# Kernel optimization log

Measured on AMD Instinct MI355X. Metric: run time of the kernel, lower is better.

Reference implementation:

```python
import jax, jax.numpy as jnp
import numpy as np

N, DX, DZ, DY, H = 8192, 64, 128, 16, 512


def setup_inputs() -> dict:
    key = jax.random.key(0)
    ks = jax.random.split(key, 8)
    s1 = 1.0 / np.sqrt(DX)
    s2 = 1.0 / np.sqrt(H)
    return {
        "z_pred": jax.random.normal(ks[0], (N, DZ), dtype=jnp.float32),
        "x_label": jax.random.normal(ks[1], (N, DX), dtype=jnp.float32),
        "y_label": jax.random.normal(ks[2], (N, DY), dtype=jnp.float32),
        "W1": jax.random.normal(ks[3], (DX, H), dtype=jnp.float32) * s1,
        "b1": jnp.zeros((H,), dtype=jnp.float32),
        "W2": jax.random.normal(ks[4], (H, DZ), dtype=jnp.float32) * s2,
        "b2": jnp.zeros((DZ,), dtype=jnp.float32),
        "A": jax.random.normal(ks[5], (DZ, DZ), dtype=jnp.float32) * (1.0 / np.sqrt(DZ)),
        "B": jax.random.normal(ks[6], (DZ, DY), dtype=jnp.float32) * (1.0 / np.sqrt(DY)),
    }


def reference(z_pred, x_label, y_label, W1, b1, W2, b2, A, B):
    # forward_mapper T: x (dx,) -> (dz,), 2-layer tanh MLP
    def T(x):
        return jnp.tanh(x @ W1 + b1) @ W2 + b2

    # diff_eq: per-sample nonlinear dynamics x_dot = tanh(x)
    x_dot = jnp.tanh(x_label)  # (N, dx)

    # per-sample Jacobian dT/dx: (N, dz, dx). Equivalent to the torch code's
    # full N x N batched Jacobian followed by the diagonal slice, but without
    # the O(N^2) waste.
    jac = jax.vmap(jax.jacrev(T))(x_label)  # (N, dz, dx)

    dtdx_mul_f = jnp.einsum("nzd,nd->nz", jac, x_dot)  # (N, dz)
    m_mul_t = z_pred @ A.T                              # (N, dz)
    k_mul_h = y_label @ B.T                             # (N, dz)

    pde = dtdx_mul_f - m_mul_t - k_mul_h                # (N, dz)
    loss_batch = jnp.linalg.norm(pde, axis=1)           # (N,)
    return jnp.mean(loss_batch)
```

## Files before the change

kernel.cpp:

```cpp
#include <hip/hip_runtime.h>
#include <math.h>

#define Nn   8192
#define DXc  64
#define DZc  128
#define DYc  16
#define Hc   512
#define KCp  672
#define SSTR 72

typedef short bf16x8 __attribute__((ext_vector_type(8)));
typedef float f32x4  __attribute__((ext_vector_type(4)));

__device__ __forceinline__ float fast_tanh(float x) {
    float e = __expf(2.0f * x);
    return 1.0f - 2.0f / (e + 1.0f);
}
__device__ __forceinline__ short f2bf(float f) {
    unsigned u = __float_as_uint(f);
    return (short)((u + 0x7FFFu + ((u >> 16) & 1u)) >> 16);
}

__global__ void prep_kernel(const float* __restrict__ W1,
                            const float* __restrict__ W2,
                            const float* __restrict__ A,
                            const float* __restrict__ Bm,
                            short* __restrict__ W1T,
                            short* __restrict__ WcT) {
    int idx = blockIdx.x * 256 + threadIdx.x;
    if (idx < Hc * DXc) {
        int j = idx >> 6, k = idx & 63;
        W1T[idx] = f2bf(W1[k * Hc + j]);
    }
    int i2 = idx - Hc * DXc;
    if (i2 >= 0 && i2 < DZc * KCp) {
        int z = i2 / KCp, k = i2 - z * KCp;
        float v = 0.f;
        if (k < Hc)                  v =  W2[k * DZc + z];
        else if (k < Hc + DZc)       v = -A[z * DZc + (k - Hc)];
        else if (k < Hc + DZc + DYc) v = -Bm[z * DYc + (k - Hc - DZc)];
        WcT[i2] = f2bf(v);
    }
}

#define MFMA16(a, b, c) __builtin_amdgcn_mfma_f32_16x16x32_bf16((a), (b), (c), 0, 0, 0)

__global__ __launch_bounds__(256, 2)
void pde_main(const float* __restrict__ z_pred,
              const float* __restrict__ x_label,
              const float* __restrict__ y_label,
              const float* __restrict__ b1,
              const short* __restrict__ W1T,
              const short* __restrict__ WcT,
              float* __restrict__ partial) {
    __shared__ __align__(16) short sS[4][16 * SSTR];
    __shared__ float Pred[4][16][DZc];
    __shared__ float rsum[16];
    __shared__ float norms[16];

    const int tid  = threadIdx.x;
    const int w    = tid >> 6;
    const int lane = tid & 63;
    const int n16  = lane & 15;
    const int q    = lane >> 4;
    const int n0   = blockIdx.x * 16;

    if (tid < 16) rsum[tid] = 0.f;

    f32x4 accP[8];
#pragma unroll
    for (int zt = 0; zt < 8; zt++) accP[zt] = (f32x4){0.f, 0.f, 0.f, 0.f};

    const float4* xr4 = (const float4*)(x_label + (size_t)(n0 + n16) * DXc + q * 8);
    float4 x0 = xr4[0], x1 = xr4[1];
    float4 x2 = xr4[8], x3 = xr4[9];
    bf16x8 ax0, ax1, at0, at1;
    {
        const float* xa = (const float*)&x0;
        float v[16] = {x0.x,x0.y,x0.z,x0.w, x1.x,x1.y,x1.z,x1.w,
                       x2.x,x2.y,x2.z,x2.w, x3.x,x3.y,x3.z,x3.w};
        (void)xa;
#pragma unroll
        for (int i = 0; i < 8; i++) {
            ax0[i] = f2bf(v[i]);                ax1[i] = f2bf(v[8 + i]);
            at0[i] = f2bf(fast_tanh(v[i]));     at1[i] = f2bf(fast_tanh(v[8 + i]));
        }
    }

    short* sw = &sS[w][0];

#pragma unroll
    for (int cc = 0; cc < 2; cc++) {
        const int jbase = (w + cc * 4) * 64;
#pragma unroll
        for (int t = 0; t < 4; t++) {
            const int jt = jbase + t * 16;
            const short* bp = W1T + (size_t)(jt + n16) * DXc + q * 8;
            bf16x8 bw0 = *(const bf16x8*)bp;
            bf16x8 bw1 = *(const bf16x8*)(bp + 32);
            f32x4 h = (f32x4){0.f, 0.f, 0.f, 0.f};
            f32x4 u = (f32x4){0.f, 0.f, 0.f, 0.f};
            h = MFMA16(ax0, bw0, h);  h = MFMA16(ax1, bw1, h);
            u = MFMA16(at0, bw0, u);  u = MFMA16(at1, bw1, u);
            const float bj = b1[jt + n16];
#pragma unroll
            for (int reg = 0; reg < 4; reg++) {
                float tv = fast_tanh(h[reg] + bj);
                float s  = (1.f - tv * tv) * u[reg];
                sw[(q * 4 + reg) * SSTR + t * 16 + n16] = f2bf(s);
            }
        }
        bf16x8 sa0 = *(const bf16x8*)(sw + n16 * SSTR + q * 8);
        bf16x8 sa1 = *(const bf16x8*)(sw + n16 * SSTR + 32 + q * 8);
#pragma unroll
        for (int zt = 0; zt < 8; zt++) {
            const short* wp = WcT + (size_t)(zt * 16 + n16) * KCp + jbase + q * 8;
            bf16x8 w0 = *(const bf16x8*)wp;
            bf16x8 w1 = *(const bf16x8*)(wp + 32);
            accP[zt] = MFMA16(sa0, w0, accP[zt]);
            accP[zt] = MFMA16(sa1, w1, accP[zt]);
        }
    }

    if (w < 2) {
        const int kz = w * 64;
        const float4* zr4 = (const float4*)(z_pred + (size_t)(n0 + n16) * DZc + kz + q * 8);
        float4 z0 = zr4[0], z1 = zr4[1], z2 = zr4[8], z3 = zr4[9];
        float v[16] = {z0.x,z0.y,z0.z,z0.w, z1.x,z1.y,z1.z,z1.w,
                       z2.x,z2.y,z2.z,z2.w, z3.x,z3.y,z3.z,z3.w};
        bf16x8 az0, az1;
#pragma unroll
        for (int i = 0; i < 8; i++) { az0[i] = f2bf(v[i]); az1[i] = f2bf(v[8 + i]); }
        const int kb = Hc + kz;
#pragma unroll
        for (int zt = 0; zt < 8; zt++) {
            const short* wp = WcT + (size_t)(zt * 16 + n16) * KCp + kb + q * 8;
            bf16x8 w0 = *(const bf16x8*)wp;
            bf16x8 w1 = *(const bf16x8*)(wp + 32);
            accP[zt] = MFMA16(az0, w0, accP[zt]);
            accP[zt] = MFMA16(az1, w1, accP[zt]);
        }
    } else if (w == 2) {
        bf16x8 ay = (bf16x8){0,0,0,0,0,0,0,0};
        if (q < 2) {
            const float4* yr4 = (const float4*)(y_label + (size_t)(n0 + n16) * DYc + q * 8);
            float4 y0 = yr4[0], y1 = yr4[1];
            float v[8] = {y0.x,y0.y,y0.z,y0.w, y1.x,y1.y,y1.z,y1.w};
#pragma unroll
            for (int i = 0; i < 8; i++) ay[i] = f2bf(v[i]);
        }
        const int kb = Hc + DZc;
#pragma unroll
        for (int zt = 0; zt < 8; zt++) {
            const short* wp = WcT + (size_t)(zt * 16 + n16) * KCp + kb + q * 8;
            bf16x8 w0 = *(const bf16x8*)wp;
            accP[zt] = MFMA16(ay, w0, accP[zt]);
        }
    }

#pragma unroll
    for (int zt = 0; zt < 8; zt++)
#pragma unroll
        for (int reg = 0; reg < 4; reg++)
            Pred[w][q * 4 + reg][zt * 16 + n16] = accP[zt][reg];
    __syncthreads();

    {
        const int r = tid & 15, seg = tid >> 4;
        float ss = 0.f;
#pragma unroll
        for (int c8 = 0; c8 < 8; c8++) {
            int c = seg * 8 + c8;
            float v = Pred[0][r][c] + Pred[1][r][c] + Pred[2][r][c] + Pred[3][r][c];
            ss = fmaf(v, v, ss);
        }
        atomicAdd(&rsum[r], ss);
    }
    __syncthreads();
    if (tid < 16) norms[tid] = sqrtf(rsum[tid]);
    __syncthreads();
    if (tid == 0) {
        float s = 0.f;
#pragma unroll
        for (int i = 0; i < 16; i++) s += norms[i];
        partial[blockIdx.x] = s;
    }
}

__global__ void reduce_kernel(const float* __restrict__ partial, float* __restrict__ out) {
    __shared__ float s4[4];
    int tid = threadIdx.x;
    float v = partial[tid] + partial[tid + 256];
#pragma unroll
    for (int off = 32; off >= 1; off >>= 1) v += __shfl_down(v, off);
    if ((tid & 63) == 0) s4[tid >> 6] = v;
    __syncthreads();
    if (tid == 0) out[0] = (s4[0] + s4[1] + s4[2] + s4[3]) * (1.0f / (float)Nn);
}

extern "C" void kernel_launch(void* const* d_in, const int* in_sizes, int n_in,
                              void* d_out, int out_size, void* d_ws, size_t ws_size,
                              hipStream_t stream) {
    const float* z_pred  = (const float*)d_in[0];
    const float* x_label = (const float*)d_in[1];
    const float* y_label = (const float*)d_in[2];
    const float* W1      = (const float*)d_in[3];
    const float* b1      = (const float*)d_in[4];
    const float* W2      = (const float*)d_in[5];
    const float* A       = (const float*)d_in[7];
    const float* Bm      = (const float*)d_in[8];

    short* W1T = (short*)d_ws;
    short* WcT = W1T + Hc * DXc;
    float* partial = (float*)(WcT + DZc * KCp);

    const int prep_elems = Hc * DXc + DZc * KCp;
    prep_kernel<<<(prep_elems + 255) / 256, 256, 0, stream>>>(W1, W2, A, Bm, W1T, WcT);
    pde_main<<<Nn / 16, 256, 0, stream>>>(z_pred, x_label, y_label, b1, W1T, WcT, partial);
    reduce_kernel<<<1, 256, 0, stream>>>(partial, (float*)d_out);
}
```

Measured before the change: 87.06 us.

## Split output columns across waves and coalesce weight prep via shared-memory transpose

The main kernel now writes the full 16x512 sensitivity tile to one shared buffer and has each wave compute a 32-column slice of the output over the full K, instead of each wave doing a K-slice over all 128 columns. This removes the 4x partial-output shared buffer and its cross-wave reduction, and replaces it with a shuffle-based row sum of squares. The prep kernel is rewritten to transpose W1/W2 through shared memory with vectorized bf16x8 stores, in 25 blocks. The trade-off is an extra block-wide barrier before the second GEMM, and every wave now reads all of sS.

```diff
diff --git a/kernel.cpp b/kernel.cpp
--- a/kernel.cpp
+++ b/kernel.cpp
@@ -7,7 +7,7 @@
 #define DYc  16
 #define Hc   512
 #define KCp  672
-#define SSTR 72
+#define SSTR 520
 
 typedef short bf16x8 __attribute__((ext_vector_type(8)));
 typedef float f32x4  __attribute__((ext_vector_type(4)));
@@ -19,6 +19,12 @@
 __device__ __forceinline__ short f2bf(float f) {
     unsigned u = __float_as_uint(f);
     return (short)((u + 0x7FFFu + ((u >> 16) & 1u)) >> 16);
+}
+__device__ __forceinline__ bf16x8 pack8(float4 a, float4 b) {
+    bf16x8 r;
+    r[0]=f2bf(a.x); r[1]=f2bf(a.y); r[2]=f2bf(a.z); r[3]=f2bf(a.w);
+    r[4]=f2bf(b.x); r[5]=f2bf(b.y); r[6]=f2bf(b.z); r[7]=f2bf(b.w);
+    return r;
 }
 
 __global__ void prep_kernel(const float* __restrict__ W1,
@@ -27,19 +33,66 @@
                             const float* __restrict__ Bm,
                             short* __restrict__ W1T,
                             short* __restrict__ WcT) {
-    int idx = blockIdx.x * 256 + threadIdx.x;
-    if (idx < Hc * DXc) {
-        int j = idx >> 6, k = idx & 63;
-        W1T[idx] = f2bf(W1[k * Hc + j]);
-    }
-    int i2 = idx - Hc * DXc;
-    if (i2 >= 0 && i2 < DZc * KCp) {
-        int z = i2 / KCp, k = i2 - z * KCp;
-        float v = 0.f;
-        if (k < Hc)                  v =  W2[k * DZc + z];
-        else if (k < Hc + DZc)       v = -A[z * DZc + (k - Hc)];
-        else if (k < Hc + DZc + DYc) v = -Bm[z * DYc + (k - Hc - DZc)];
-        WcT[i2] = f2bf(v);
+    __shared__ float tile[64 * 129];
+    const int blk = blockIdx.x, t = threadIdx.x;
+
+    if (blk < 8) {
+        const int jb = blk * 64;
+#pragma unroll
+        for (int p = 0; p < 16; p++) {
+            int lin = p * 256 + t;
+            int k = lin >> 6, jj = lin & 63;
+            tile[jj * 65 + k] = W1[(size_t)k * Hc + jb + jj];
+        }
+        __syncthreads();
+#pragma unroll
+        for (int p = 0; p < 2; p++) {
+            int jj = p * 32 + (t >> 3), k8 = (t & 7) * 8;
+            bf16x8 v;
+#pragma unroll
+            for (int i = 0; i < 8; i++) v[i] = f2bf(tile[jj * 65 + k8 + i]);
+            *(bf16x8*)(W1T + (size_t)(jb + jj) * DXc + k8) = v;
+        }
+    } else if (blk < 16) {
+        const int kb = (blk - 8) * 64;
+#pragma unroll
+        for (int p = 0; p < 32; p++) {
+            int lin = p * 256 + t;
+            int kk = lin >> 7, z = lin & 127;
+            tile[kk * 129 + z] = W2[(size_t)(kb + kk) * DZc + z];
+        }
+        __syncthreads();
+#pragma unroll
+        for (int p = 0; p < 4; p++) {
+            int z = p * 32 + (t >> 3), k8 = (t & 7) * 8;
+            bf16x8 v;
+#pragma unroll
+            for (int i = 0; i < 8; i++) v[i] = f2bf(tile[(k8 + i) * 129 + z]);
+            *(bf16x8*)(WcT + (size_t)z * KCp + kb + k8) = v;
+        }
+    } else if (blk < 24) {
+        int idx8 = (blk - 16) * 256 + t;
+        int z = idx8 >> 4, c8 = (idx8 & 15) * 8;
+        float4 a0 = *(const float4*)(A + (size_t)z * DZc + c8);
+        float4 a1 = *(const float4*)(A + (size_t)z * DZc + c8 + 4);
+        bf16x8 v;
+        v[0]=f2bf(-a0.x); v[1]=f2bf(-a0.y); v[2]=f2bf(-a0.z); v[3]=f2bf(-a0.w);
+        v[4]=f2bf(-a1.x); v[5]=f2bf(-a1.y); v[6]=f2bf(-a1.z); v[7]=f2bf(-a1.w);
+        *(bf16x8*)(WcT + (size_t)z * KCp + Hc + c8) = v;
+    } else {
+#pragma unroll
+        for (int p = 0; p < 2; p++) {
+            int cid = p * 256 + t;
+            int z = cid >> 2, c8 = (cid & 3) * 8;
+            bf16x8 v = (bf16x8){0,0,0,0,0,0,0,0};
+            if (c8 < DYc) {
+                float4 b0 = *(const float4*)(Bm + (size_t)z * DYc + c8);
+                float4 b1 = *(const float4*)(Bm + (size_t)z * DYc + c8 + 4);
+                v[0]=f2bf(-b0.x); v[1]=f2bf(-b0.y); v[2]=f2bf(-b0.z); v[3]=f2bf(-b0.w);
+                v[4]=f2bf(-b1.x); v[5]=f2bf(-b1.y); v[6]=f2bf(-b1.z); v[7]=f2bf(-b1.w);
+            }
+            *(bf16x8*)(WcT + (size_t)z * KCp + Hc + DZc + c8) = v;
+        }
     }
 }
 
@@ -53,10 +106,8 @@
               const short* __restrict__ W1T,
               const short* __restrict__ WcT,
               float* __restrict__ partial) {
-    __shared__ __align__(16) short sS[4][16 * SSTR];
-    __shared__ float Pred[4][16][DZc];
+    __shared__ __align__(16) short sS[16 * SSTR];
     __shared__ float rsum[16];
-    __shared__ float norms[16];
 
     const int tid  = threadIdx.x;
     const int w    = tid >> 6;
@@ -67,39 +118,29 @@
 
     if (tid < 16) rsum[tid] = 0.f;
 
-    f32x4 accP[8];
-#pragma unroll
-    for (int zt = 0; zt < 8; zt++) accP[zt] = (f32x4){0.f, 0.f, 0.f, 0.f};
-
-    const float4* xr4 = (const float4*)(x_label + (size_t)(n0 + n16) * DXc + q * 8);
-    float4 x0 = xr4[0], x1 = xr4[1];
-    float4 x2 = xr4[8], x3 = xr4[9];
-    bf16x8 ax0, ax1, at0, at1;
+    const float* xp = x_label + (size_t)(n0 + n16) * DXc + q * 8;
+    float4 x0 = *(const float4*)xp,        x1 = *(const float4*)(xp + 4);
+    float4 x2 = *(const float4*)(xp + 32), x3 = *(const float4*)(xp + 36);
+    bf16x8 ax0 = pack8(x0, x1), ax1 = pack8(x2, x3);
+    bf16x8 at0, at1;
     {
-        const float* xa = (const float*)&x0;
         float v[16] = {x0.x,x0.y,x0.z,x0.w, x1.x,x1.y,x1.z,x1.w,
                        x2.x,x2.y,x2.z,x2.w, x3.x,x3.y,x3.z,x3.w};
-        (void)xa;
-#pragma unroll
-        for (int i = 0; i < 8; i++) {
-            ax0[i] = f2bf(v[i]);                ax1[i] = f2bf(v[8 + i]);
-            at0[i] = f2bf(fast_tanh(v[i]));     at1[i] = f2bf(fast_tanh(v[8 + i]));
-        }
-    }
-
-    short* sw = &sS[w][0];
+#pragma unroll
+        for (int i = 0; i < 8; i++) { at0[i] = f2bf(fast_tanh(v[i])); at1[i] = f2bf(fast_tanh(v[8 + i])); }
+    }
 
 #pragma unroll
     for (int cc = 0; cc < 2; cc++) {
-        const int jbase = (w + cc * 4) * 64;
+        const int jb = w * 128 + cc * 64;
 #pragma unroll
         for (int t = 0; t < 4; t++) {
-            const int jt = jbase + t * 16;
+            const int jt = jb + t * 16;
             const short* bp = W1T + (size_t)(jt + n16) * DXc + q * 8;
             bf16x8 bw0 = *(const bf16x8*)bp;
             bf16x8 bw1 = *(const bf16x8*)(bp + 32);
-            f32x4 h = (f32x4){0.f, 0.f, 0.f, 0.f};
-            f32x4 u = (f32x4){0.f, 0.f, 0.f, 0.f};
+            f32x4 h = (f32x4){0.f,0.f,0.f,0.f};
+            f32x4 u = (f32x4){0.f,0.f,0.f,0.f};
             h = MFMA16(ax0, bw0, h);  h = MFMA16(ax1, bw1, h);
             u = MFMA16(at0, bw0, u);  u = MFMA16(at1, bw1, u);
             const float bj = b1[jt + n16];
@@ -107,82 +148,73 @@
             for (int reg = 0; reg < 4; reg++) {
                 float tv = fast_tanh(h[reg] + bj);
                 float s  = (1.f - tv * tv) * u[reg];
-                sw[(q * 4 + reg) * SSTR + t * 16 + n16] = f2bf(s);
+                sS[(q * 4 + reg) * SSTR + jt + n16] = f2bf(s);
             }
         }
-        bf16x8 sa0 = *(const bf16x8*)(sw + n16 * SSTR + q * 8);
-        bf16x8 sa1 = *(const bf16x8*)(sw + n16 * SSTR + 32 + q * 8);
-#pragma unroll
-        for (int zt = 0; zt < 8; zt++) {
-            const short* wp = WcT + (size_t)(zt * 16 + n16) * KCp + jbase + q * 8;
-            bf16x8 w0 = *(const bf16x8*)wp;
-            bf16x8 w1 = *(const bf16x8*)(wp + 32);
-            accP[zt] = MFMA16(sa0, w0, accP[zt]);
-            accP[zt] = MFMA16(sa1, w1, accP[zt]);
-        }
-    }
-
-    if (w < 2) {
-        const int kz = w * 64;
-        const float4* zr4 = (const float4*)(z_pred + (size_t)(n0 + n16) * DZc + kz + q * 8);
-        float4 z0 = zr4[0], z1 = zr4[1], z2 = zr4[8], z3 = zr4[9];
-        float v[16] = {z0.x,z0.y,z0.z,z0.w, z1.x,z1.y,z1.z,z1.w,
-                       z2.x,z2.y,z2.z,z2.w, z3.x,z3.y,z3.z,z3.w};
-        bf16x8 az0, az1;
-#pragma unroll
-        for (int i = 0; i < 8; i++) { az0[i] = f2bf(v[i]); az1[i] = f2bf(v[8 + i]); }
-        const int kb = Hc + kz;
-#pragma unroll
-        for (int zt = 0; zt < 8; zt++) {
-            const short* wp = WcT + (size_t)(zt * 16 + n16) * KCp + kb + q * 8;
-            bf16x8 w0 = *(const bf16x8*)wp;
-            bf16x8 w1 = *(const bf16x8*)(wp + 32);
-            accP[zt] = MFMA16(az0, w0, accP[zt]);
-            accP[zt] = MFMA16(az1, w1, accP[zt]);
-        }
-    } else if (w == 2) {
+    }
+
+    const int z0r = w * 32;
+    const short* wr0 = WcT + (size_t)(z0r + n16) * KCp;
+    const short* wr1 = WcT + (size_t)(z0r + 16 + n16) * KCp;
+    f32x4 acc0 = (f32x4){0.f,0.f,0.f,0.f};
+    f32x4 acc1 = (f32x4){0.f,0.f,0.f,0.f};
+
+    {
+        const float* zp = z_pred + (size_t)(n0 + n16) * DZc + q * 8;
+#pragma unroll
+        for (int kc = 0; kc < 4; kc++) {
+            float4 a0 = *(const float4*)(zp + kc * 32);
+            float4 a1 = *(const float4*)(zp + kc * 32 + 4);
+            bf16x8 az = pack8(a0, a1);
+            bf16x8 b0 = *(const bf16x8*)(wr0 + Hc + kc * 32 + q * 8);
+            bf16x8 b1f = *(const bf16x8*)(wr1 + Hc + kc * 32 + q * 8);
+            acc0 = MFMA16(az, b0, acc0);
+            acc1 = MFMA16(az, b1f, acc1);
+        }
+    }
+    {
         bf16x8 ay = (bf16x8){0,0,0,0,0,0,0,0};
         if (q < 2) {
-            const float4* yr4 = (const float4*)(y_label + (size_t)(n0 + n16) * DYc + q * 8);
-            float4 y0 = yr4[0], y1 = yr4[1];
-            float v[8] = {y0.x,y0.y,y0.z,y0.w, y1.x,y1.y,y1.z,y1.w};
-#pragma unroll
-            for (int i = 0; i < 8; i++) ay[i] = f2bf(v[i]);
-        }
-        const int kb = Hc + DZc;
-#pragma unroll
-        for (int zt = 0; zt < 8; zt++) {
-            const short* wp = WcT + (size_t)(zt * 16 + n16) * KCp + kb + q * 8;
-            bf16x8 w0 = *(const bf16x8*)wp;
-            accP[zt] = MFMA16(ay, w0, accP[zt]);
-        }
-    }
-
-#pragma unroll
-    for (int zt = 0; zt < 8; zt++)
-#pragma unroll
-        for (int reg = 0; reg < 4; reg++)
-            Pred[w][q * 4 + reg][zt * 16 + n16] = accP[zt][reg];
+            const float* yp = y_label + (size_t)(n0 + n16) * DYc + q * 8;
+            float4 y0 = *(const float4*)yp, y1 = *(const float4*)(yp + 4);
+            ay = pack8(y0, y1);
+        }
+        bf16x8 b0 = *(const bf16x8*)(wr0 + Hc + DZc + q * 8);
+        bf16x8 b1f = *(const bf16x8*)(wr1 + Hc + DZc + q * 8);
+        acc0 = MFMA16(ay, b0, acc0);
+        acc1 = MFMA16(ay, b1f, acc1);
+    }
+
     __syncthreads();
 
-    {
-        const int r = tid & 15, seg = tid >> 4;
-        float ss = 0.f;
-#pragma unroll
-        for (int c8 = 0; c8 < 8; c8++) {
-            int c = seg * 8 + c8;
-            float v = Pred[0][r][c] + Pred[1][r][c] + Pred[2][r][c] + Pred[3][r][c];
-            ss = fmaf(v, v, ss);
-        }
-        atomicAdd(&rsum[r], ss);
+#pragma unroll
+    for (int kc = 0; kc < 16; kc++) {
+        bf16x8 sa = *(const bf16x8*)(sS + n16 * SSTR + kc * 32 + q * 8);
+        bf16x8 b0 = *(const bf16x8*)(wr0 + kc * 32 + q * 8);
+        bf16x8 b1f = *(const bf16x8*)(wr1 + kc * 32 + q * 8);
+        acc0 = MFMA16(sa, b0, acc0);
+        acc1 = MFMA16(sa, b1f, acc1);
+    }
+
+    float ss[4];
+#pragma unroll
+    for (int reg = 0; reg < 4; reg++) {
+        ss[reg] = fmaf(acc0[reg], acc0[reg], acc1[reg] * acc1[reg]);
+        ss[reg] += __shfl_xor(ss[reg], 1);
+        ss[reg] += __shfl_xor(ss[reg], 2);
+        ss[reg] += __shfl_xor(ss[reg], 4);
+        ss[reg] += __shfl_xor(ss[reg], 8);
+    }
+    if (n16 == 0) {
+#pragma unroll
+        for (int reg = 0; reg < 4; reg++) atomicAdd(&rsum[q * 4 + reg], ss[reg]);
     }
     __syncthreads();
-    if (tid < 16) norms[tid] = sqrtf(rsum[tid]);
-    __syncthreads();
+
     if (tid == 0) {
         float s = 0.f;
 #pragma unroll
-        for (int i = 0; i < 16; i++) s += norms[i];
+        for (int i = 0; i < 16; i++) s += sqrtf(rsum[i]);
         partial[blockIdx.x] = s;
     }
 }
@@ -214,8 +246,7 @@
     short* WcT = W1T + Hc * DXc;
     float* partial = (float*)(WcT + DZc * KCp);
 
-    const int prep_elems = Hc * DXc + DZc * KCp;
-    prep_kernel<<<(prep_elems + 255) / 256, 256, 0, stream>>>(W1, W2, A, Bm, W1T, WcT);
+    prep_kernel<<<25, 256, 0, stream>>>(W1, W2, A, Bm, W1T, WcT);
     pde_main<<<Nn / 16, 256, 0, stream>>>(z_pred, x_label, y_label, b1, W1T, WcT, partial);
     reduce_kernel<<<1, 256, 0, stream>>>(partial, (float*)d_out);
 }
```

Result: slower. 89.23 us (+2.5%).
